# Kernel optimization log

Measured on AMD Instinct MI355X. Metric: run time of the kernel, lower is better.

The kernel has to match this reference:

```python
import jax, jax.numpy as jnp
import numpy as np

VARIANCE = 1.0
MASK_SCORE = -1e15
LOG_2PI = float(np.log(2.0 * np.pi))


def setup_inputs() -> dict:
    key = jax.random.key(0)
    k1, k2, k3 = jax.random.split(key, 3)
    B, N, H, T = 16, 512, 512, 4096
    inputs = jax.random.normal(k1, (B, N, H), dtype=jnp.float32)
    # positive durations; mean ~ T/N so cumulative centers span the output frames
    durations = jax.random.uniform(k2, (B, N), dtype=jnp.float32) * (2.0 * T / N)
    inputs_len = jax.random.randint(k3, (B,), N // 2, N + 1).astype(jnp.int64)
    return {"inputs": inputs, "inputs_len": inputs_len,
            "durations": durations, "output_max_len": T}


def reference(inputs, inputs_len, durations, output_max_len):
    # inputs: [B,N,H], durations: [B,N], inputs_len: [B] -> out [B,T,H]
    var = jnp.asarray(VARIANCE, dtype=jnp.float32)
    c = jnp.cumsum(durations, axis=1) - 0.5 * durations          # [B,N] gaussian centers
    t = jnp.arange(output_max_len, dtype=jnp.float32)            # [T]
    # log-gaussian scores [B,N,T]
    w_t = -0.5 * (LOG_2PI + jnp.log(var)
                  + jnp.square(t[None, None, :] - c[:, :, None]) / var)
    # mask out padded phoneme positions (n >= inputs_len)
    valid = jnp.arange(durations.shape[1])[None, :] < inputs_len[:, None]  # [B,N]
    w_t = jnp.where(valid[:, :, None], w_t, MASK_SCORE)
    w_t = jax.nn.softmax(w_t, axis=1)                            # softmax over N
    # weighted sum: out[b,t,h] = sum_n w_t[b,n,t] * inputs[b,n,h]
    return jnp.einsum('bnt,bnh->bth', w_t, inputs)
```

## Files before the change

### kernel.cpp

```cpp
#include <hip/hip_runtime.h>
#include <math.h>

#define WIN 16
#define THRESH 20.0f
#define FPW 8
#define NW  4
#define FPB (FPW * NW)
#define CH  16

#define AS1 __attribute__((address_space(1)))
#define AS3 __attribute__((address_space(3)))

__global__ void centers_kernel(const float* __restrict__ dur,
                               float* __restrict__ c, int N) {
    extern __shared__ double s[];
    int b = blockIdx.x;
    int n = threadIdx.x;
    float d = (n < N) ? dur[(size_t)b * N + n] : 0.0f;
    if (n < N) s[n] = (double)d;
    __syncthreads();
    for (int off = 1; off < N; off <<= 1) {
        double v = (n >= off && n < N) ? s[n - off] : 0.0;
        __syncthreads();
        if (n < N) s[n] += v;
        __syncthreads();
    }
    if (n < N) c[(size_t)b * N + n] = (float)(s[n] - 0.5 * (double)d);
}

__global__ __launch_bounds__(256) void bounds_kernel(
    const float* __restrict__ c, const int* __restrict__ lens,
    int* __restrict__ pack, float* __restrict__ marr,
    float* __restrict__ inv, int N, int T) {
    int gt = blockIdx.x * 256 + threadIdx.x;
    int b = gt / T;
    int t = gt - b * T;
    const float* cb = c + (size_t)b * N;
    int L = lens[b];
    if (L < 1) L = 1;
    if (L > N) L = N;
    float tf = (float)t;
    int lo = 0, hi = L;
    while (lo < hi) {
        int mid = (lo + hi) >> 1;
        if (cb[mid] < tf) lo = mid + 1; else hi = mid;
    }
    int j = lo;
    if (j >= L) j = L - 1;
    float cj   = cb[j];
    float cjm1 = cb[(j > 0) ? (j - 1) : 0];
    if (j > 0 && (tf - cjm1) < (cj - tf)) j--;
    float dm = tf - cb[j];
    float m = -0.5f * dm * dm;
    float lim = m - THRESH;
    int aCap = j - WIN; if (aCap < 0) aCap = 0;
    int eCap = j + WIN; if (eCap > L - 1) eCap = L - 1;
    int a = j, e = j;
    while (a > aCap) {
        float d = tf - cb[a - 1];
        if (-0.5f * d * d >= lim) --a; else break;
    }
    while (e < eCap) {
        float d = tf - cb[e + 1];
        if (-0.5f * d * d >= lim) ++e; else break;
    }
    float sum = 0.0f;
    for (int k = a; k <= e; ++k) {
        float d  = tf - cb[k];
        float sc = -0.5f * d * d;
        sum += __expf(sc - m);
    }
    pack[gt] = a | ((e - a + 1) << 16);
    marr[gt] = m;
    inv[gt]  = 1.0f / sum;
}

__global__ __launch_bounds__(256, 4) void upsample_rl(
    const float* __restrict__ x,
    const float* __restrict__ c,
    const int* __restrict__ pack,
    const float* __restrict__ marr,
    const float* __restrict__ inv,
    float* __restrict__ out,
    int B, int N, int H, int T) {
    __shared__ float rows[CH][512];
    __shared__ int   bmin[NW], bmax[NW];

    int nwg = gridDim.x;
    int bid = blockIdx.x;
    if ((nwg & 7) == 0) {
        int cpx = nwg >> 3;
        bid = (bid & 7) * cpx + (bid >> 3);
    }
    int wave = threadIdx.x >> 6;
    int lane = threadIdx.x & 63;

    int tilesPerB = T / FPB;
    int b   = bid / tilesPerB;
    int t0  = (bid - b * tilesPerB) * FPB + wave * FPW;

    const float* cb = c + (size_t)b * N;

    const int*   pb  = pack + (size_t)b * T + t0;
    const float* mb  = marr + (size_t)b * T + t0;
    const float* ivb = inv  + (size_t)b * T + t0;
    float tf[FPW], m_[FPW], iv[FPW];
    int a[FPW], K[FPW];
    int amin = 0x7fffffff, emax = 0;
    #pragma unroll
    for (int f = 0; f < FPW; ++f) {
        tf[f] = (float)(t0 + f);
        int pk = pb[f];
        a[f] = pk & 0xffff;
        K[f] = pk >> 16;
        m_[f] = mb[f];
        iv[f] = ivb[f];
        int ef = a[f] + K[f] - 1;
        if (a[f] < amin) amin = a[f];
        if (ef > emax)   emax = ef;
    }

    if (lane == 0) { bmin[wave] = amin; bmax[wave] = emax; }
    __syncthreads();
    int n0 = min(min(bmin[0], bmin[1]), min(bmin[2], bmin[3]));
    int ne = max(max(bmax[0], bmax[1]), max(bmax[2], bmax[3]));
    int span = ne - n0 + 1;

    const float* gbase = x + ((size_t)b * N + n0) * (size_t)H;

    float4 acc[FPW][2];
    #pragma unroll
    for (int f = 0; f < FPW; ++f) {
        acc[f][0] = make_float4(0.f, 0.f, 0.f, 0.f);
        acc[f][1] = make_float4(0.f, 0.f, 0.f, 0.f);
    }

    for (int kb = 0; kb < span; kb += CH) {
        int klen = span - kb; if (klen > CH) klen = CH;

        for (int r = wave; r < klen; r += NW) {
            const char* g = (const char*)(gbase + (size_t)(kb + r) * H);
            __builtin_amdgcn_global_load_lds(
                (const AS1 void*)(g + lane * 16),
                (AS3 void*)&rows[r][0], 16, 0, 0);
            __builtin_amdgcn_global_load_lds(
                (const AS1 void*)(g + 1024 + lane * 16),
                (AS3 void*)&rows[r][256], 16, 0, 0);
        }

        int nidx = n0 + kb + lane;
        int ci = nidx; if (ci > N - 1) ci = N - 1;
        float cv = cb[ci];
        float wv[FPW];
        #pragma unroll
        for (int f = 0; f < FPW; ++f) {
            float d  = tf[f] - cv;
            float wval = __expf(-0.5f * d * d - m_[f]) * iv[f];
            unsigned q = (unsigned)(nidx - a[f]);
            wv[f] = (q < (unsigned)K[f]) ? wval : 0.0f;
        }
        __syncthreads();

        for (int k = 0; k < klen; ++k) {
            float wk[FPW];
            #pragma unroll
            for (int f = 0; f < FPW; ++f)
                wk[f] = __uint_as_float(
                    __builtin_amdgcn_readlane(__float_as_uint(wv[f]), k));
            const float4* row = (const float4*)rows[k];
            float4 va = row[lane];
            float4 vb = row[64 + lane];
            #pragma unroll
            for (int f = 0; f < FPW; ++f) {
                acc[f][0].x = fmaf(wk[f], va.x, acc[f][0].x);
                acc[f][0].y = fmaf(wk[f], va.y, acc[f][0].y);
                acc[f][0].z = fmaf(wk[f], va.z, acc[f][0].z);
                acc[f][0].w = fmaf(wk[f], va.w, acc[f][0].w);
                acc[f][1].x = fmaf(wk[f], vb.x, acc[f][1].x);
                acc[f][1].y = fmaf(wk[f], vb.y, acc[f][1].y);
                acc[f][1].z = fmaf(wk[f], vb.z, acc[f][1].z);
                acc[f][1].w = fmaf(wk[f], vb.w, acc[f][1].w);
            }
        }
        __syncthreads();
    }

    float* obase = out + ((size_t)b * T + t0) * (size_t)H;
    #pragma unroll
    for (int f = 0; f < FPW; ++f) {
        float4* o = (float4*)(obase + (size_t)f * H);
        o[lane]      = acc[f][0];
        o[64 + lane] = acc[f][1];
    }
}

extern "C" void kernel_launch(void* const* d_in, const int* in_sizes, int n_in,
                              void* d_out, int out_size, void* d_ws, size_t ws_size,
                              hipStream_t stream) {
    const float* x    = (const float*)d_in[0];
    const int*   lens = (const int*)d_in[1];
    const float* dur  = (const float*)d_in[2];

    int B  = in_sizes[1];
    int BN = in_sizes[2];
    int N  = BN / B;
    int H  = in_sizes[0] / BN;
    int T  = out_size / (B * H);

    size_t cB  = (size_t)B * N * sizeof(float);
    size_t btB = (size_t)B * T * sizeof(int);

    float* c   = (float*)d_ws;
    int*   pk  = (int*)((char*)d_ws + cB);
    float* mar = (float*)((char*)pk + btB);
    float* ivr = (float*)((char*)mar + btB);

    centers_kernel<<<B, N, N * sizeof(double), stream>>>(dur, c, N);
    bounds_kernel<<<(B * T) / 256, 256, 0, stream>>>(c, lens, pk, mar, ivr, N, T);

    int blocks = (B * T) / FPB;
    upsample_rl<<<blocks, 256, 0, stream>>>(x, c, pk, mar, ivr,
                                            (float*)d_out, B, N, H, T);
}
```

Baseline: 39.86 us.

## Load input rows directly into registers per wave instead of staging in LDS

Removes the shared-memory staging of input rows and the block-wide barriers. Each wave now computes its own span of phonemes and streams rows from global memory straight into registers, using a two-row register prefetch pipeline. This drops LDS traffic and synchronisation, and lets the per-wave span be tighter than the block-wide union. The cost is that the four waves may fetch overlapping rows redundantly through cache, and the live registers for the prefetched rows may raise register pressure.

```diff
diff --git a/kernel.cpp b/kernel.cpp
--- a/kernel.cpp
+++ b/kernel.cpp
@@ -6,10 +6,6 @@
 #define FPW 8
 #define NW  4
 #define FPB (FPW * NW)
-#define CH  16
-
-#define AS1 __attribute__((address_space(1)))
-#define AS3 __attribute__((address_space(3)))
 
 __global__ void centers_kernel(const float* __restrict__ dur,
                                float* __restrict__ c, int N) {
@@ -75,7 +71,7 @@
     inv[gt]  = 1.0f / sum;
 }
 
-__global__ __launch_bounds__(256, 4) void upsample_rl(
+__global__ __launch_bounds__(256, 4) void upsample_direct(
     const float* __restrict__ x,
     const float* __restrict__ c,
     const int* __restrict__ pack,
@@ -83,9 +79,6 @@
     const float* __restrict__ inv,
     float* __restrict__ out,
     int B, int N, int H, int T) {
-    __shared__ float rows[CH][512];
-    __shared__ int   bmin[NW], bmax[NW];
-
     int nwg = gridDim.x;
     int bid = blockIdx.x;
     if ((nwg & 7) == 0) {
@@ -104,12 +97,11 @@
     const int*   pb  = pack + (size_t)b * T + t0;
     const float* mb  = marr + (size_t)b * T + t0;
     const float* ivb = inv  + (size_t)b * T + t0;
-    float tf[FPW], m_[FPW], iv[FPW];
+    float m_[FPW], iv[FPW];
     int a[FPW], K[FPW];
     int amin = 0x7fffffff, emax = 0;
     #pragma unroll
     for (int f = 0; f < FPW; ++f) {
-        tf[f] = (float)(t0 + f);
         int pk = pb[f];
         a[f] = pk & 0xffff;
         K[f] = pk >> 16;
@@ -119,14 +111,10 @@
         if (a[f] < amin) amin = a[f];
         if (ef > emax)   emax = ef;
     }
-
-    if (lane == 0) { bmin[wave] = amin; bmax[wave] = emax; }
-    __syncthreads();
-    int n0 = min(min(bmin[0], bmin[1]), min(bmin[2], bmin[3]));
-    int ne = max(max(bmax[0], bmax[1]), max(bmax[2], bmax[3]));
-    int span = ne - n0 + 1;
-
-    const float* gbase = x + ((size_t)b * N + n0) * (size_t)H;
+    int span = emax - amin + 1;
+
+    const float4* rbase = (const float4*)(x + ((size_t)b * N + amin) * (size_t)H);
+    int H4 = H >> 2;
 
     float4 acc[FPW][2];
     #pragma unroll
@@ -135,54 +123,50 @@
         acc[f][1] = make_float4(0.f, 0.f, 0.f, 0.f);
     }
 
-    for (int kb = 0; kb < span; kb += CH) {
-        int klen = span - kb; if (klen > CH) klen = CH;
-
-        for (int r = wave; r < klen; r += NW) {
-            const char* g = (const char*)(gbase + (size_t)(kb + r) * H);
-            __builtin_amdgcn_global_load_lds(
-                (const AS1 void*)(g + lane * 16),
-                (AS3 void*)&rows[r][0], 16, 0, 0);
-            __builtin_amdgcn_global_load_lds(
-                (const AS1 void*)(g + 1024 + lane * 16),
-                (AS3 void*)&rows[r][256], 16, 0, 0);
-        }
-
-        int nidx = n0 + kb + lane;
+    for (int kb = 0; kb < span; kb += 64) {
+        int klen = span - kb; if (klen > 64) klen = 64;
+
+        int nidx = amin + kb + lane;
         int ci = nidx; if (ci > N - 1) ci = N - 1;
         float cv = cb[ci];
         float wv[FPW];
         #pragma unroll
         for (int f = 0; f < FPW; ++f) {
-            float d  = tf[f] - cv;
+            float d  = (float)(t0 + f) - cv;
             float wval = __expf(-0.5f * d * d - m_[f]) * iv[f];
             unsigned q = (unsigned)(nidx - a[f]);
             wv[f] = (q < (unsigned)K[f]) ? wval : 0.0f;
         }
-        __syncthreads();
-
+
+        const float4* rp = rbase + (size_t)kb * H4;
+        float4 va0, vb0, va1, vb1;
+        va0 = rp[lane]; vb0 = rp[64 + lane];
+        if (klen > 1) { va1 = rp[H4 + lane]; vb1 = rp[H4 + 64 + lane]; }
         for (int k = 0; k < klen; ++k) {
+            float4 na, nb;
+            if (k + 2 < klen) {
+                const float4* rn = rp + (size_t)(k + 2) * H4;
+                na = rn[lane]; nb = rn[64 + lane];
+            }
             float wk[FPW];
             #pragma unroll
             for (int f = 0; f < FPW; ++f)
                 wk[f] = __uint_as_float(
                     __builtin_amdgcn_readlane(__float_as_uint(wv[f]), k));
-            const float4* row = (const float4*)rows[k];
-            float4 va = row[lane];
-            float4 vb = row[64 + lane];
             #pragma unroll
             for (int f = 0; f < FPW; ++f) {
-                acc[f][0].x = fmaf(wk[f], va.x, acc[f][0].x);
-                acc[f][0].y = fmaf(wk[f], va.y, acc[f][0].y);
-                acc[f][0].z = fmaf(wk[f], va.z, acc[f][0].z);
-                acc[f][0].w = fmaf(wk[f], va.w, acc[f][0].w);
-                acc[f][1].x = fmaf(wk[f], vb.x, acc[f][1].x);
-                acc[f][1].y = fmaf(wk[f], vb.y, acc[f][1].y);
-                acc[f][1].z = fmaf(wk[f], vb.z, acc[f][1].z);
-                acc[f][1].w = fmaf(wk[f], vb.w, acc[f][1].w);
+                acc[f][0].x = fmaf(wk[f], va0.x, acc[f][0].x);
+                acc[f][0].y = fmaf(wk[f], va0.y, acc[f][0].y);
+                acc[f][0].z = fmaf(wk[f], va0.z, acc[f][0].z);
+                acc[f][0].w = fmaf(wk[f], va0.w, acc[f][0].w);
+                acc[f][1].x = fmaf(wk[f], vb0.x, acc[f][1].x);
+                acc[f][1].y = fmaf(wk[f], vb0.y, acc[f][1].y);
+                acc[f][1].z = fmaf(wk[f], vb0.z, acc[f][1].z);
+                acc[f][1].w = fmaf(wk[f], vb0.w, acc[f][1].w);
             }
+            va0 = va1; vb0 = vb1;
+            va1 = na;  vb1 = nb;
         }
-        __syncthreads();
     }
 
     float* obase = out + ((size_t)b * T + t0) * (size_t)H;
@@ -219,6 +203,6 @@
     bounds_kernel<<<(B * T) / 256, 256, 0, stream>>>(c, lens, pk, mar, ivr, N, T);
 
     int blocks = (B * T) / FPB;
-    upsample_rl<<<blocks, 256, 0, stream>>>(x, c, pk, mar, ivr,
-                                            (float*)d_out, B, N, H, T);
-}
+    upsample_direct<<<blocks, 256, 0, stream>>>(x, c, pk, mar, ivr,
+                                                (float*)d_out, B, N, H, T);
+}
```

After: 58.00 us. 45.5% more time.

## Fuse center prefix-sum and bounds computation into one prep kernel, pack per-frame params

Applied to the files above, without the earlier changes.

Merges the centers scan and the per-frame bounds search into one kernel. Each block recomputes the batch's prefix sum in shared memory and runs its binary search on LDS instead of global memory. The per-frame window start, length, max score and inverse sum are packed into one float4 so the main kernel does a single vector load per frame. This removes one launch and the global round-trip for centers, at the cost of redundant scans across blocks. The new prep kernel also hardcodes N=512 (two elements per thread) and assumes T is a multiple of 256.

```diff
diff --git a/kernel.cpp b/kernel.cpp
--- a/kernel.cpp
+++ b/kernel.cpp
@@ -11,76 +11,82 @@
 #define AS1 __attribute__((address_space(1)))
 #define AS3 __attribute__((address_space(3)))
 
-__global__ void centers_kernel(const float* __restrict__ dur,
-                               float* __restrict__ c, int N) {
-    extern __shared__ double s[];
-    int b = blockIdx.x;
-    int n = threadIdx.x;
-    float d = (n < N) ? dur[(size_t)b * N + n] : 0.0f;
-    if (n < N) s[n] = (double)d;
+__global__ __launch_bounds__(256) void prep_kernel(
+    const float* __restrict__ dur, const int* __restrict__ lens,
+    float* __restrict__ c, float4* __restrict__ pm, int N, int T) {
+    __shared__ double s[512];
+    __shared__ float cf[512];
+    int tpc = T >> 8;
+    int b   = blockIdx.x / tpc;
+    int tc  = blockIdx.x - b * tpc;
+    int tid = threadIdx.x;
+
+    int n0 = tid, n1 = tid + 256;
+    float d0 = dur[(size_t)b * N + n0];
+    float d1 = dur[(size_t)b * N + n1];
+    s[n0] = (double)d0; s[n1] = (double)d1;
     __syncthreads();
     for (int off = 1; off < N; off <<= 1) {
-        double v = (n >= off && n < N) ? s[n - off] : 0.0;
-        __syncthreads();
-        if (n < N) s[n] += v;
-        __syncthreads();
-    }
-    if (n < N) c[(size_t)b * N + n] = (float)(s[n] - 0.5 * (double)d);
-}
-
-__global__ __launch_bounds__(256) void bounds_kernel(
-    const float* __restrict__ c, const int* __restrict__ lens,
-    int* __restrict__ pack, float* __restrict__ marr,
-    float* __restrict__ inv, int N, int T) {
-    int gt = blockIdx.x * 256 + threadIdx.x;
-    int b = gt / T;
-    int t = gt - b * T;
-    const float* cb = c + (size_t)b * N;
+        double v0 = (n0 >= off) ? s[n0 - off] : 0.0;
+        double v1 = (n1 >= off) ? s[n1 - off] : 0.0;
+        __syncthreads();
+        s[n0] += v0; s[n1] += v1;
+        __syncthreads();
+    }
+    cf[n0] = (float)(s[n0] - 0.5 * (double)d0);
+    cf[n1] = (float)(s[n1] - 0.5 * (double)d1);
+    __syncthreads();
+    if (tc == 0) {
+        c[(size_t)b * N + n0] = cf[n0];
+        c[(size_t)b * N + n1] = cf[n1];
+    }
+
     int L = lens[b];
     if (L < 1) L = 1;
     if (L > N) L = N;
+    int t = tc * 256 + tid;
     float tf = (float)t;
     int lo = 0, hi = L;
     while (lo < hi) {
         int mid = (lo + hi) >> 1;
-        if (cb[mid] < tf) lo = mid + 1; else hi = mid;
+        if (cf[mid] < tf) lo = mid + 1; else hi = mid;
     }
     int j = lo;
     if (j >= L) j = L - 1;
-    float cj   = cb[j];
-    float cjm1 = cb[(j > 0) ? (j - 1) : 0];
+    float cj   = cf[j];
+    float cjm1 = cf[(j > 0) ? (j - 1) : 0];
     if (j > 0 && (tf - cjm1) < (cj - tf)) j--;
-    float dm = tf - cb[j];
+    float dm = tf - cf[j];
     float m = -0.5f * dm * dm;
     float lim = m - THRESH;
     int aCap = j - WIN; if (aCap < 0) aCap = 0;
     int eCap = j + WIN; if (eCap > L - 1) eCap = L - 1;
     int a = j, e = j;
     while (a > aCap) {
-        float d = tf - cb[a - 1];
+        float d = tf - cf[a - 1];
         if (-0.5f * d * d >= lim) --a; else break;
     }
     while (e < eCap) {
-        float d = tf - cb[e + 1];
+        float d = tf - cf[e + 1];
         if (-0.5f * d * d >= lim) ++e; else break;
     }
     float sum = 0.0f;
     for (int k = a; k <= e; ++k) {
-        float d  = tf - cb[k];
-        float sc = -0.5f * d * d;
-        sum += __expf(sc - m);
-    }
-    pack[gt] = a | ((e - a + 1) << 16);
-    marr[gt] = m;
-    inv[gt]  = 1.0f / sum;
+        float d = tf - cf[k];
+        sum += __expf(-0.5f * d * d - m);
+    }
+    float4 o;
+    o.x = __uint_as_float((unsigned)(a | ((e - a + 1) << 16)));
+    o.y = m;
+    o.z = 1.0f / sum;
+    o.w = 0.0f;
+    pm[(size_t)b * T + t] = o;
 }
 
 __global__ __launch_bounds__(256, 4) void upsample_rl(
     const float* __restrict__ x,
     const float* __restrict__ c,
-    const int* __restrict__ pack,
-    const float* __restrict__ marr,
-    const float* __restrict__ inv,
+    const float4* __restrict__ pm,
     float* __restrict__ out,
     int B, int N, int H, int T) {
     __shared__ float rows[CH][512];
@@ -101,20 +107,19 @@
 
     const float* cb = c + (size_t)b * N;
 
-    const int*   pb  = pack + (size_t)b * T + t0;
-    const float* mb  = marr + (size_t)b * T + t0;
-    const float* ivb = inv  + (size_t)b * T + t0;
+    const float4* pmb = pm + (size_t)b * T + t0;
     float tf[FPW], m_[FPW], iv[FPW];
     int a[FPW], K[FPW];
     int amin = 0x7fffffff, emax = 0;
     #pragma unroll
     for (int f = 0; f < FPW; ++f) {
         tf[f] = (float)(t0 + f);
-        int pk = pb[f];
-        a[f] = pk & 0xffff;
-        K[f] = pk >> 16;
-        m_[f] = mb[f];
-        iv[f] = ivb[f];
+        float4 p = pmb[f];
+        unsigned pk = __float_as_uint(p.x);
+        a[f] = (int)(pk & 0xffffu);
+        K[f] = (int)(pk >> 16);
+        m_[f] = p.y;
+        iv[f] = p.z;
         int ef = a[f] + K[f] - 1;
         if (a[f] < amin) amin = a[f];
         if (ef > emax)   emax = ef;
@@ -207,18 +212,15 @@
     int H  = in_sizes[0] / BN;
     int T  = out_size / (B * H);
 
-    size_t cB  = (size_t)B * N * sizeof(float);
-    size_t btB = (size_t)B * T * sizeof(int);
-
-    float* c   = (float*)d_ws;
-    int*   pk  = (int*)((char*)d_ws + cB);
-    float* mar = (float*)((char*)pk + btB);
-    float* ivr = (float*)((char*)mar + btB);
-
-    centers_kernel<<<B, N, N * sizeof(double), stream>>>(dur, c, N);
-    bounds_kernel<<<(B * T) / 256, 256, 0, stream>>>(c, lens, pk, mar, ivr, N, T);
+    size_t cB = (size_t)B * N * sizeof(float);
+    cB = (cB + 15) & ~(size_t)15;
+
+    float*  c  = (float*)d_ws;
+    float4* pm = (float4*)((char*)d_ws + cB);
+
+    prep_kernel<<<B * (T >> 8), 256, 0, stream>>>(dur, lens, c, pm, N, T);
 
     int blocks = (B * T) / FPB;
-    upsample_rl<<<blocks, 256, 0, stream>>>(x, c, pk, mar, ivr,
-                                            (float*)d_out, B, N, H, T);
+    upsample_rl<<<blocks, 256, 0, stream>>>(x, c, pm, (float*)d_out,
+                                            B, N, H, T);
 }
```

Result: faster. 35.48 us (median of 2 runs) (-11.0%).
